# Kernel tuning notes

Hardware: AMD Instinct MI355X
Metric: run time of the kernel (lower is better)

The kernel has to match this reference:

```python
import jax, jax.numpy as jnp
import numpy as np

B, S, HID, H = 1, 4096, 1024, 16
D = HID // H  # 64
SCALE = D ** -0.5
NEG = -1e30


def setup_inputs() -> dict:
    key = jax.random.key(0)
    ks = jax.random.split(key, 8)
    hidden_states = jax.random.normal(ks[0], (B, S, HID), dtype=jnp.float32)
    attention_mask = jax.random.randint(ks[1], (B, S), 0, 2, dtype=jnp.int32)
    # Linear weights stored as [in, out] so y = x @ W + b
    init = lambda k, shape: jax.random.normal(k, shape, dtype=jnp.float32) * (HID ** -0.5)
    return {
        "hidden_states": hidden_states,
        "attention_mask": attention_mask,
        "Wq": init(ks[2], (HID, HID)), "bq": jnp.zeros((HID,), jnp.float32),
        "Wk": init(ks[3], (HID, HID)), "bk": jnp.zeros((HID,), jnp.float32),
        "Wv": init(ks[4], (HID, HID)), "bv": jnp.zeros((HID,), jnp.float32),
    }


def reference(hidden_states, attention_mask, Wq, bq, Wk, bk, Wv, bv):
    x = hidden_states
    q = (x @ Wq + bq).reshape(B, S, H, D)
    k = (x @ Wk + bk).reshape(B, S, H, D)
    v = (x @ Wv + bv).reshape(B, S, H, D)
    mask = attention_mask.astype(bool)  # [B, S] over keys
    # scores: [B, H, Sq, Sk]
    scores = jnp.einsum("bqhd,bkhd->bhqk", q, k) * SCALE
    scores = jnp.where(mask[:, None, None, :], scores, NEG)
    attn = jax.nn.softmax(scores, axis=-1)
    ctx = jnp.einsum("bhqk,bkhd->bqhd", attn, v).reshape(B, S, HID)
    return (ctx,)
```

## Files before the change

### kernel.cpp

```cpp
#include <hip/hip_runtime.h>
#include <stdint.h>

#define S_    4096
#define HID_  1024
#define H_    16
#define N3    3072
#define NT    64
#define SCALE_f 0.125f
#define NEG_f  (-1e30f)
#define SCL2  (0.125f * 1.44269504089f)
#define THRRAW 44.3614f

typedef __attribute__((ext_vector_type(4))) float f32x4;
typedef __attribute__((ext_vector_type(8))) short bf16x8;
typedef __attribute__((ext_vector_type(4))) short bf16x4;

#define MFMA16(a,b,c) __builtin_amdgcn_mfma_f32_16x16x32_bf16((a),(b),(c),0,0,0)
#define GLDS16(g,l) __builtin_amdgcn_global_load_lds( \
    (__attribute__((address_space(1))) void*)(g), \
    (__attribute__((address_space(3))) void*)(l), 16, 0, 0)

__device__ __forceinline__ f32x4 MFMA16K16(bf16x4 a, bf16x4 b, f32x4 c){
#if __has_builtin(__builtin_amdgcn_mfma_f32_16x16x16bf16_1k)
  return __builtin_amdgcn_mfma_f32_16x16x16bf16_1k(a, b, c, 0, 0, 0);
#else
  asm volatile("v_mfma_f32_16x16x16_bf16 %0, %1, %2, %0" : "+v"(c) : "v"(a), "v"(b));
  return c;
#endif
}

__device__ __forceinline__ float max3f(float a, float b, float c){
  float d; asm("v_max3_f32 %0, %1, %2, %3" : "=v"(d) : "v"(a), "v"(b), "v"(c)); return d;
}
__device__ __forceinline__ uint32_t cvtpk(float lo, float hi){
  uint32_t r; asm("v_cvt_pk_bf16_f32 %0, %1, %2" : "=v"(r) : "v"(lo), "v"(hi)); return r;
}

__device__ __forceinline__ unsigned short f2b(float f){
  union { float f; uint32_t u; } a; a.f = f;
  uint32_t u = a.u;
  return (unsigned short)((u + 0x7fffu + ((u >> 16) & 1u)) >> 16);
}

__global__ __launch_bounds__(256) void cvt_x_kern(const float* __restrict__ x,
                                                  unsigned short* __restrict__ xb){
  int i = (blockIdx.x * 256 + threadIdx.x) * 4;
  const float4 v = *(const float4*)(x + i);
  ushort4 o;
  o.x = f2b(v.x); o.y = f2b(v.y); o.z = f2b(v.z); o.w = f2b(v.w);
  *(ushort4*)(xb + i) = o;
}

__global__ __launch_bounds__(256) void cvt_w_t_kern(const float* __restrict__ W,
                                                    unsigned short* __restrict__ wt,
                                                    int nbase){
  __shared__ float tile[32][33];
  int k0 = blockIdx.x * 32, n0 = blockIdx.y * 32;
  int tx = threadIdx.x, ty = threadIdx.y;
  for (int i = 0; i < 32; i += 8)
    tile[ty + i][tx] = W[(k0 + ty + i) * HID_ + n0 + tx];
  __syncthreads();
  for (int i = 0; i < 32; i += 8)
    wt[(nbase + n0 + ty + i) * HID_ + k0 + tx] = f2b(tile[tx][ty + i]);
}

#define BM 128
#define BN 128
#define BK 32
__global__ __launch_bounds__(256) void gemm_qkv_kern(
    const unsigned short* __restrict__ xb,
    const unsigned short* __restrict__ wt,
    const float* __restrict__ bq, const float* __restrict__ bk,
    const float* __restrict__ bv,
    unsigned short* __restrict__ qkv)
{
  __shared__ unsigned short As[BM * BK];
  __shared__ unsigned short Bs[BN * BK];
  int tid = threadIdx.x;
  int lane = tid & 63, wid = tid >> 6;
  int g = lane >> 4, l16 = lane & 15;
  int m0 = blockIdx.x * BM, n0 = blockIdx.y * BN;
  int wm = (wid >> 1) * 64, wn = (wid & 1) * 64;

  f32x4 acc[4][4];
  f32x4 z = {0.f, 0.f, 0.f, 0.f};
  for (int mi = 0; mi < 4; mi++) for (int ni = 0; ni < 4; ni++) acc[mi][ni] = z;

  for (int kt = 0; kt < HID_; kt += BK) {
    __syncthreads();
    for (int i = 0; i < 2; i++) {
      int flat = tid * 8 + i * 2048;
      int m = flat >> 5, k = flat & 31;
      GLDS16(xb + (m0 + m) * HID_ + kt + k, As + flat);
    }
    for (int i = 0; i < 2; i++) {
      int flat = tid * 8 + i * 2048;
      int n = flat >> 5, k = flat & 31;
      GLDS16(wt + (n0 + n) * HID_ + kt + k, Bs + flat);
    }
    __syncthreads();
    bf16x8 a[4], b[4];
    for (int mi = 0; mi < 4; mi++)
      a[mi] = *(const bf16x8*)(As + (wm + mi * 16 + l16) * BK + g * 8);
    for (int ni = 0; ni < 4; ni++)
      b[ni] = *(const bf16x8*)(Bs + (wn + ni * 16 + l16) * BK + g * 8);
    for (int mi = 0; mi < 4; mi++)
      for (int ni = 0; ni < 4; ni++)
        acc[mi][ni] = MFMA16(a[mi], b[ni], acc[mi][ni]);
  }

  for (int mi = 0; mi < 4; mi++)
    for (int ni = 0; ni < 4; ni++) {
      int col = n0 + wn + ni * 16 + l16;
      float bias = (col < 1024) ? bq[col] : ((col < 2048) ? bk[col - 1024] : bv[col - 2048]);
      for (int r = 0; r < 4; r++) {
        int row = m0 + wm + mi * 16 + g * 4 + r;
        qkv[row * N3 + col] = f2b(acc[mi][ni][r] + bias);
      }
    }
}

__global__ __launch_bounds__(256) void vt_kern(const unsigned short* __restrict__ qkv,
                                               const int* __restrict__ mask,
                                               unsigned short* __restrict__ vt){
  __shared__ unsigned short tl[64][72];
  int h = blockIdx.y, k0 = blockIdx.x * 64, tid = threadIdx.x;
  int key = tid >> 2, dq = (tid & 3) * 16;
  const unsigned short* src = qkv + (size_t)(k0 + key) * N3 + 2048 + h * 64 + dq;
  bf16x8 v0 = *(const bf16x8*)src;
  bf16x8 v1 = *(const bf16x8*)(src + 8);
  if (mask[k0 + key] == 0) {
    bf16x8 zz = {0,0,0,0,0,0,0,0};
    v0 = zz; v1 = zz;
  }
  *(bf16x8*)&tl[key][dq]     = v0;
  *(bf16x8*)&tl[key][dq + 8] = v1;
  __syncthreads();
  int d = tid >> 2, kq = (tid & 3) * 16;
  unsigned short* dst = vt + ((size_t)h * 64 + d) * S_ + k0 + kq;
  bf16x8 o0, o1;
  for (int j = 0; j < 8; j++) { o0[j] = tl[kq + j][d]; o1[j] = tl[kq + 8 + j][d]; }
  *(bf16x8*)dst = o0; *(bf16x8*)(dst + 8) = o1;
}

__global__ void maskbits_kern(const int* __restrict__ mask,
                              unsigned long long* __restrict__ mb){
  int t = threadIdx.x;
  unsigned long long wv = 0;
  for (int j = 0; j < 64; j++)
    wv |= (unsigned long long)(mask[t * 64 + j] != 0) << j;
  mb[t] = wv;
}

__global__ __launch_bounds__(256, 4) void attn_kern(
    const unsigned short* __restrict__ qkv,
    const unsigned short* __restrict__ vt,
    const unsigned long long* __restrict__ mb,
    float* __restrict__ out)
{
  __shared__ unsigned short Ks[2][64 * 64];
  __shared__ unsigned short Vs[2][64 * 64];
  __shared__ unsigned long long MaskL[NT];

  int tid = threadIdx.x, lane = tid & 63, w = tid >> 6;
  int g = lane >> 4, l16 = lane & 15;
  int bid = blockIdx.x;
  int swz = (bid & 7) * 128 + (bid >> 3);
  int h = swz >> 6, q0 = (swz & 63) * 64;

  const unsigned short* Q = qkv + h * 64;
  const unsigned short* K = qkv + 1024 + h * 64;
  const unsigned short* V = vt + (size_t)h * 64 * S_;

  if (tid < NT) MaskL[tid] = mb[tid];

  bf16x8 qf[2];
  for (int ks = 0; ks < 2; ks++)
    qf[ks] = *(const bf16x8*)(Q + (size_t)(q0 + w * 16 + l16) * N3 + ks * 32 + g * 8);

  f32x4 po[4];
  f32x4 z = {0.f, 0.f, 0.f, 0.f};
  for (int db = 0; db < 4; db++) po[db] = z;
  float m_l = -__builtin_inff(), l_l = 0.f;

  int swl = (l16 & 7) << 4;
  int rof[2];
  for (int ks = 0; ks < 2; ks++) rof[ks] = ((ks * 64 + g * 16) ^ swl) >> 1;
  int vof[4];
  for (int nb = 0; nb < 4; nb++) vof[nb] = ((nb * 32 + g * 8) ^ swl) >> 1;

  auto STAGE = [&](int b, int t) {
    int k0 = t * 64;
    for (int i = 0; i < 2; i++) {
      int F = tid * 16 + i * 4096;
      int row = F >> 7, inner = F & 127;
      int sin = (inner ^ ((row & 7) << 4)) >> 1;
      GLDS16(K + (size_t)(k0 + row) * N3 + sin, &Ks[b][F >> 1]);
      GLDS16(V + (size_t)row * S_ + k0 + sin,    &Vs[b][F >> 1]);
    }
  };

  STAGE(0, 0);
  asm volatile("s_waitcnt vmcnt(0) lgkmcnt(0)" ::: "memory");
  __builtin_amdgcn_s_barrier();

  int cur = 0;
  for (int t = 0; t < NT; t++) {
    if (t + 1 < NT) STAGE(cur ^ 1, t + 1);
    unsigned long long mw = MaskL[t];
    uint32_t mlo = (uint32_t)mw, mhi = (uint32_t)(mw >> 32);

    f32x4 sc[4];
    for (int nb = 0; nb < 4; nb++) sc[nb] = z;
    for (int nb = 0; nb < 4; nb++) {
      int rb = (nb * 16 + l16) * 64;
      for (int ks = 0; ks < 2; ks++) {
        bf16x8 kf = *(const bf16x8*)(&Ks[cur][rb + rof[ks]]);
        sc[nb] = MFMA16(kf, qf[ks], sc[nb]);
      }
    }

    float m0 = max3f(sc[0][0], sc[0][1], sc[0][2]);
    float m1 = max3f(sc[0][3], sc[1][0], sc[1][1]);
    float m2 = max3f(sc[1][2], sc[1][3], sc[2][0]);
    float m3 = max3f(sc[2][1], sc[2][2], sc[2][3]);
    float m4 = max3f(sc[3][0], sc[3][1], sc[3][2]);
    float m5 = max3f(m0, m1, sc[3][3]);
    float m6 = max3f(m2, m3, m4);
    float pmax = fmaxf(m5, m6);
    pmax = fmaxf(pmax, __shfl_xor(pmax, 16, 64));
    pmax = fmaxf(pmax, __shfl_xor(pmax, 32, 64));

    if (__ballot(pmax > m_l + THRRAW)) {
      float mnew = fmaxf(m_l, pmax);
      float alpha = __builtin_amdgcn_exp2f((m_l - mnew) * SCL2);
      for (int db = 0; db < 4; db++) po[db] *= alpha;
      l_l *= alpha;
      m_l = mnew;
    }
    float negmsc = m_l * (-SCL2);

    float rsum = 0.f;
    bf16x4 pb[4];
    for (int nb = 0; nb < 4; nb++) {
      uint32_t msrc = (nb < 2) ? mlo : mhi;
      float pr[4];
      for (int r = 0; r < 4; r++) {
        float p = __builtin_amdgcn_exp2f(__builtin_fmaf(sc[nb][r], SCL2, negmsc));
        float b = (float)((msrc >> ((nb & 1) * 16 + g * 4 + r)) & 1u);
        rsum = __builtin_fmaf(p, b, rsum);
        pr[r] = p;
      }
      union { uint32_t w[2]; bf16x4 v; } pu;
      pu.w[0] = cvtpk(pr[0], pr[1]);
      pu.w[1] = cvtpk(pr[2], pr[3]);
      pb[nb] = pu.v;
    }
    rsum += __shfl_xor(rsum, 16, 64);
    rsum += __shfl_xor(rsum, 32, 64);
    l_l += rsum;

    for (int db = 0; db < 4; db++) {
      int rb = (db * 16 + l16) * 64;
      for (int nb = 0; nb < 4; nb++) {
        bf16x4 va = *(const bf16x4*)(&Vs[cur][rb + vof[nb]]);
        po[db] = MFMA16K16(va, pb[nb], po[db]);
      }
    }

    asm volatile("s_waitcnt vmcnt(0) lgkmcnt(0)" ::: "memory");
    __builtin_amdgcn_s_barrier();
    cur ^= 1;
  }

  float inv = 1.0f / l_l;
  int q = q0 + w * 16 + l16;
  for (int db = 0; db < 4; db++) {
    f32x4 v = po[db] * inv;
    *(f32x4*)(out + (size_t)q * HID_ + h * 64 + db * 16 + g * 4) = v;
  }
}

extern "C" void kernel_launch(void* const* d_in, const int* in_sizes, int n_in,
                              void* d_out, int out_size, void* d_ws, size_t ws_size,
                              hipStream_t stream) {
  const float* x    = (const float*)d_in[0];
  const int*   mask = (const int*)d_in[1];
  const float* Wq   = (const float*)d_in[2];
  const float* bq   = (const float*)d_in[3];
  const float* Wk   = (const float*)d_in[4];
  const float* bk   = (const float*)d_in[5];
  const float* Wv   = (const float*)d_in[6];
  const float* bv   = (const float*)d_in[7];
  float* out = (float*)d_out;

  uint8_t* ws = (uint8_t*)d_ws;
  unsigned short* xb  = (unsigned short*)ws;
  unsigned short* wt  = (unsigned short*)(ws + (8u  << 20));
  unsigned short* qkv = (unsigned short*)(ws + (14u << 20));
  unsigned short* vt  = (unsigned short*)ws;
  unsigned long long* mb = (unsigned long long*)(ws + (8u << 20));

  cvt_x_kern<<<(S_ * HID_) / (256 * 4), 256, 0, stream>>>(x, xb);
  dim3 tg(HID_ / 32, HID_ / 32);
  cvt_w_t_kern<<<tg, dim3(32, 8), 0, stream>>>(Wq, wt, 0);
  cvt_w_t_kern<<<tg, dim3(32, 8), 0, stream>>>(Wk, wt, 1024);
  cvt_w_t_kern<<<tg, dim3(32, 8), 0, stream>>>(Wv, wt, 2048);
  gemm_qkv_kern<<<dim3(S_ / BM, N3 / BN), 256, 0, stream>>>(xb, wt, bq, bk, bv, qkv);
  vt_kern<<<dim3(S_ / 64, H_), 256, 0, stream>>>(qkv, mask, vt);
  maskbits_kern<<<1, 64, 0, stream>>>(mask, mb);
  attn_kern<<<S_ / 64 * H_, 256, 0, stream>>>(qkv, vt, mb, out);
}
```

Before: 261.8 us.

## Zero masked keys upfront, subtract masked count from row sum, process 128 queries per block

Masked keys now have their K rows zeroed in vt_kern, so their score is exactly zero and their exp contribution is exp(-m). The per-element mask bit extraction is replaced by one per-tile correction that subtracts count*exp2(-m*scale) from the row sum. Each wave also handles two 16-query groups, so every K/V fragment read from LDS is reused twice and the grid is halved. The cost is more registers (launch bounds lowered to 2 blocks per CU) and fewer blocks. The subtraction correction may lose precision when masked terms dominate the sum.

```diff
diff --git a/kernel.cpp b/kernel.cpp
--- a/kernel.cpp
+++ b/kernel.cpp
@@ -120,18 +120,20 @@
     }
 }
 
-__global__ __launch_bounds__(256) void vt_kern(const unsigned short* __restrict__ qkv,
+__global__ __launch_bounds__(256) void vt_kern(unsigned short* __restrict__ qkv,
                                                const int* __restrict__ mask,
                                                unsigned short* __restrict__ vt){
   __shared__ unsigned short tl[64][72];
   int h = blockIdx.y, k0 = blockIdx.x * 64, tid = threadIdx.x;
   int key = tid >> 2, dq = (tid & 3) * 16;
-  const unsigned short* src = qkv + (size_t)(k0 + key) * N3 + 2048 + h * 64 + dq;
+  unsigned short* src = qkv + (size_t)(k0 + key) * N3 + 2048 + h * 64 + dq;
   bf16x8 v0 = *(const bf16x8*)src;
   bf16x8 v1 = *(const bf16x8*)(src + 8);
   if (mask[k0 + key] == 0) {
     bf16x8 zz = {0,0,0,0,0,0,0,0};
     v0 = zz; v1 = zz;
+    unsigned short* kdst = qkv + (size_t)(k0 + key) * N3 + 1024 + h * 64 + dq;
+    *(bf16x8*)kdst = zz; *(bf16x8*)(kdst + 8) = zz;
   }
   *(bf16x8*)&tl[key][dq]     = v0;
   *(bf16x8*)&tl[key][dq + 8] = v1;
@@ -143,45 +145,46 @@
   *(bf16x8*)dst = o0; *(bf16x8*)(dst + 8) = o1;
 }
 
-__global__ void maskbits_kern(const int* __restrict__ mask,
-                              unsigned long long* __restrict__ mb){
+__global__ void maskcnt_kern(const int* __restrict__ mask,
+                             float* __restrict__ mc){
   int t = threadIdx.x;
-  unsigned long long wv = 0;
-  for (int j = 0; j < 64; j++)
-    wv |= (unsigned long long)(mask[t * 64 + j] != 0) << j;
-  mb[t] = wv;
-}
-
-__global__ __launch_bounds__(256, 4) void attn_kern(
+  int c = 0;
+  for (int j = 0; j < 64; j++) c += (mask[t * 64 + j] == 0);
+  mc[t] = (float)c;
+}
+
+__global__ __launch_bounds__(256, 2) void attn_kern(
     const unsigned short* __restrict__ qkv,
     const unsigned short* __restrict__ vt,
-    const unsigned long long* __restrict__ mb,
+    const float* __restrict__ mc,
     float* __restrict__ out)
 {
   __shared__ unsigned short Ks[2][64 * 64];
   __shared__ unsigned short Vs[2][64 * 64];
-  __shared__ unsigned long long MaskL[NT];
+  __shared__ float MaskC[NT];
 
   int tid = threadIdx.x, lane = tid & 63, w = tid >> 6;
   int g = lane >> 4, l16 = lane & 15;
   int bid = blockIdx.x;
-  int swz = (bid & 7) * 128 + (bid >> 3);
-  int h = swz >> 6, q0 = (swz & 63) * 64;
+  int swz = (bid & 7) * 64 + (bid >> 3);
+  int h = swz >> 5, q0 = (swz & 31) * 128;
 
   const unsigned short* Q = qkv + h * 64;
   const unsigned short* K = qkv + 1024 + h * 64;
   const unsigned short* V = vt + (size_t)h * 64 * S_;
 
-  if (tid < NT) MaskL[tid] = mb[tid];
-
-  bf16x8 qf[2];
-  for (int ks = 0; ks < 2; ks++)
-    qf[ks] = *(const bf16x8*)(Q + (size_t)(q0 + w * 16 + l16) * N3 + ks * 32 + g * 8);
-
-  f32x4 po[4];
+  if (tid < NT) MaskC[tid] = mc[tid];
+
+  bf16x8 qf[2][2];
+  for (int j = 0; j < 2; j++)
+    for (int ks = 0; ks < 2; ks++)
+      qf[j][ks] = *(const bf16x8*)(Q + (size_t)(q0 + w * 32 + j * 16 + l16) * N3 + ks * 32 + g * 8);
+
+  f32x4 po[2][4];
   f32x4 z = {0.f, 0.f, 0.f, 0.f};
-  for (int db = 0; db < 4; db++) po[db] = z;
-  float m_l = -__builtin_inff(), l_l = 0.f;
+  for (int j = 0; j < 2; j++) for (int db = 0; db < 4; db++) po[j][db] = z;
+  float m_l[2] = {-__builtin_inff(), -__builtin_inff()};
+  float l_l[2] = {0.f, 0.f};
 
   int swl = (l16 & 7) << 4;
   int rof[2];
@@ -207,64 +210,65 @@
   int cur = 0;
   for (int t = 0; t < NT; t++) {
     if (t + 1 < NT) STAGE(cur ^ 1, t + 1);
-    unsigned long long mw = MaskL[t];
-    uint32_t mlo = (uint32_t)mw, mhi = (uint32_t)(mw >> 32);
-
-    f32x4 sc[4];
-    for (int nb = 0; nb < 4; nb++) sc[nb] = z;
-    for (int nb = 0; nb < 4; nb++) {
-      int rb = (nb * 16 + l16) * 64;
-      for (int ks = 0; ks < 2; ks++) {
-        bf16x8 kf = *(const bf16x8*)(&Ks[cur][rb + rof[ks]]);
-        sc[nb] = MFMA16(kf, qf[ks], sc[nb]);
-      }
-    }
-
-    float m0 = max3f(sc[0][0], sc[0][1], sc[0][2]);
-    float m1 = max3f(sc[0][3], sc[1][0], sc[1][1]);
-    float m2 = max3f(sc[1][2], sc[1][3], sc[2][0]);
-    float m3 = max3f(sc[2][1], sc[2][2], sc[2][3]);
-    float m4 = max3f(sc[3][0], sc[3][1], sc[3][2]);
-    float m5 = max3f(m0, m1, sc[3][3]);
-    float m6 = max3f(m2, m3, m4);
-    float pmax = fmaxf(m5, m6);
-    pmax = fmaxf(pmax, __shfl_xor(pmax, 16, 64));
-    pmax = fmaxf(pmax, __shfl_xor(pmax, 32, 64));
-
-    if (__ballot(pmax > m_l + THRRAW)) {
-      float mnew = fmaxf(m_l, pmax);
-      float alpha = __builtin_amdgcn_exp2f((m_l - mnew) * SCL2);
-      for (int db = 0; db < 4; db++) po[db] *= alpha;
-      l_l *= alpha;
-      m_l = mnew;
-    }
-    float negmsc = m_l * (-SCL2);
-
-    float rsum = 0.f;
-    bf16x4 pb[4];
-    for (int nb = 0; nb < 4; nb++) {
-      uint32_t msrc = (nb < 2) ? mlo : mhi;
-      float pr[4];
-      for (int r = 0; r < 4; r++) {
-        float p = __builtin_amdgcn_exp2f(__builtin_fmaf(sc[nb][r], SCL2, negmsc));
-        float b = (float)((msrc >> ((nb & 1) * 16 + g * 4 + r)) & 1u);
-        rsum = __builtin_fmaf(p, b, rsum);
-        pr[r] = p;
-      }
-      union { uint32_t w[2]; bf16x4 v; } pu;
-      pu.w[0] = cvtpk(pr[0], pr[1]);
-      pu.w[1] = cvtpk(pr[2], pr[3]);
-      pb[nb] = pu.v;
-    }
-    rsum += __shfl_xor(rsum, 16, 64);
-    rsum += __shfl_xor(rsum, 32, 64);
-    l_l += rsum;
+    float cf = MaskC[t];
+
+    bf16x4 pb[2][4];
+    for (int j = 0; j < 2; j++) {
+      f32x4 sc[4];
+      for (int nb = 0; nb < 4; nb++) sc[nb] = z;
+      for (int nb = 0; nb < 4; nb++) {
+        int rb = (nb * 16 + l16) * 64;
+        for (int ks = 0; ks < 2; ks++) {
+          bf16x8 kf = *(const bf16x8*)(&Ks[cur][rb + rof[ks]]);
+          sc[nb] = MFMA16(kf, qf[j][ks], sc[nb]);
+        }
+      }
+
+      float m0 = max3f(sc[0][0], sc[0][1], sc[0][2]);
+      float m1 = max3f(sc[0][3], sc[1][0], sc[1][1]);
+      float m2 = max3f(sc[1][2], sc[1][3], sc[2][0]);
+      float m3 = max3f(sc[2][1], sc[2][2], sc[2][3]);
+      float m4 = max3f(sc[3][0], sc[3][1], sc[3][2]);
+      float m5 = max3f(m0, m1, sc[3][3]);
+      float m6 = max3f(m2, m3, m4);
+      float pmax = fmaxf(m5, m6);
+      pmax = fmaxf(pmax, __shfl_xor(pmax, 16, 64));
+      pmax = fmaxf(pmax, __shfl_xor(pmax, 32, 64));
+
+      if (__ballot(pmax > m_l[j] + THRRAW)) {
+        float mnew = fmaxf(m_l[j], pmax);
+        float alpha = __builtin_amdgcn_exp2f((m_l[j] - mnew) * SCL2);
+        for (int db = 0; db < 4; db++) po[j][db] *= alpha;
+        l_l[j] *= alpha;
+        m_l[j] = mnew;
+      }
+      float negmsc = m_l[j] * (-SCL2);
+
+      float rsum = 0.f;
+      for (int nb = 0; nb < 4; nb++) {
+        float pr[4];
+        for (int r = 0; r < 4; r++) {
+          float p = __builtin_amdgcn_exp2f(__builtin_fmaf(sc[nb][r], SCL2, negmsc));
+          rsum += p;
+          pr[r] = p;
+        }
+        union { uint32_t wd[2]; bf16x4 v; } pu;
+        pu.wd[0] = cvtpk(pr[0], pr[1]);
+        pu.wd[1] = cvtpk(pr[2], pr[3]);
+        pb[j][nb] = pu.v;
+      }
+      rsum += __shfl_xor(rsum, 16, 64);
+      rsum += __shfl_xor(rsum, 32, 64);
+      float p0 = __builtin_amdgcn_exp2f(negmsc);
+      l_l[j] += __builtin_fmaf(-cf, p0, rsum);
+    }
 
     for (int db = 0; db < 4; db++) {
       int rb = (db * 16 + l16) * 64;
       for (int nb = 0; nb < 4; nb++) {
         bf16x4 va = *(const bf16x4*)(&Vs[cur][rb + vof[nb]]);
-        po[db] = MFMA16K16(va, pb[nb], po[db]);
+        po[0][db] = MFMA16K16(va, pb[0][nb], po[0][db]);
+        po[1][db] = MFMA16K16(va, pb[1][nb], po[1][db]);
       }
     }
 
@@ -273,11 +277,13 @@
     cur ^= 1;
   }
 
-  float inv = 1.0f / l_l;
-  int q = q0 + w * 16 + l16;
-  for (int db = 0; db < 4; db++) {
-    f32x4 v = po[db] * inv;
-    *(f32x4*)(out + (size_t)q * HID_ + h * 64 + db * 16 + g * 4) = v;
+  for (int j = 0; j < 2; j++) {
+    float inv = 1.0f / l_l[j];
+    int q = q0 + w * 32 + j * 16 + l16;
+    for (int db = 0; db < 4; db++) {
+      f32x4 v = po[j][db] * inv;
+      *(f32x4*)(out + (size_t)q * HID_ + h * 64 + db * 16 + g * 4) = v;
+    }
   }
 }
 
@@ -299,7 +305,7 @@
   unsigned short* wt  = (unsigned short*)(ws + (8u  << 20));
   unsigned short* qkv = (unsigned short*)(ws + (14u << 20));
   unsigned short* vt  = (unsigned short*)ws;
-  unsigned long long* mb = (unsigned long long*)(ws + (8u << 20));
+  float* mc = (float*)(ws + (8u << 20));
 
   cvt_x_kern<<<(S_ * HID_) / (256 * 4), 256, 0, stream>>>(x, xb);
   dim3 tg(HID_ / 32, HID_ / 32);
@@ -308,6 +314,6 @@
   cvt_w_t_kern<<<tg, dim3(32, 8), 0, stream>>>(Wv, wt, 2048);
   gemm_qkv_kern<<<dim3(S_ / BM, N3 / BN), 256, 0, stream>>>(xb, wt, bq, bk, bv, qkv);
   vt_kern<<<dim3(S_ / 64, H_), 256, 0, stream>>>(qkv, mask, vt);
-  maskbits_kern<<<1, 64, 0, stream>>>(mask, mb);
-  attn_kern<<<S_ / 64 * H_, 256, 0, stream>>>(qkv, vt, mb, out);
-}
+  maskcnt_kern<<<1, 64, 0, stream>>>(mask, mc);
+  attn_kern<<<(S_ / 128) * H_, 256, 0, stream>>>(qkv, vt, mc, out);
+}
```

Measured after the change: 255.6 us. 2.4% less time.
